# Optimization experiments

Hardware: AMD Instinct MI355X
Metric: run time of the kernel (lower is better)

The kernel has to match this reference:

```python
import jax, jax.numpy as jnp
import numpy as np

B, S, DM = 1, 4096, 2048
H, HD = 16, 128
TS = 16          # tile_size
TOPK = 16        # anchor tiles per query
NUM_TILES = S // TS


def setup_inputs() -> dict:
    key = jax.random.key(0)
    ks = jax.random.split(key, 7)
    x = jax.random.normal(ks[0], (B, S, DM), jnp.float32)
    Wq = jax.random.normal(ks[1], (DM, H * HD), jnp.float32) * 0.02
    Wk = jax.random.normal(ks[2], (DM, H * HD), jnp.float32) * 0.02
    Wv = jax.random.normal(ks[3], (DM, H * HD), jnp.float32) * 0.02
    Wo = jax.random.normal(ks[4], (H * HD, DM), jnp.float32) * 0.02
    # RoPE angles: pos * inv_freq, shape [S, HD//2] (= freqs_cis angle)
    inv_freq = 1.0 / (10000.0 ** (np.arange(0, HD, 2, dtype=np.float32) / HD))
    freqs = jnp.asarray(np.arange(S, dtype=np.float32)[:, None] * inv_freq[None, :])
    anchor_indices = jax.random.randint(ks[5], (B, H, S, TOPK), 0, NUM_TILES).astype(jnp.int32)
    return {"x": x, "Wq": Wq, "Wk": Wk, "Wv": Wv, "Wo": Wo,
            "freqs": freqs, "anchor_indices": anchor_indices}


def _rotate_half(z):
    half = z.shape[-1] // 2
    return jnp.concatenate([-z[..., half:], z[..., :half]], axis=-1)


def reference(x, Wq, Wk, Wv, Wo, freqs, anchor_indices):
    b, s, _ = x.shape
    num_tiles = s // TS
    # QKV projections -> [B, H, S, HD]
    q = (x @ Wq).reshape(b, s, H, HD).transpose(0, 2, 1, 3)
    k = (x @ Wk).reshape(b, s, H, HD).transpose(0, 2, 1, 3)
    v = (x @ Wv).reshape(b, s, H, HD).transpose(0, 2, 1, 3)
    # RoPE (half-split / rotate_half convention), float32
    cos = jnp.cos(freqs)[None, None, :s, :]
    sin = jnp.sin(freqs)[None, None, :s, :]
    cos_full = jnp.concatenate([cos, cos], axis=-1)
    sin_full = jnp.concatenate([sin, sin], axis=-1)
    q = q * cos_full + _rotate_half(q) * sin_full
    k = k * cos_full + _rotate_half(k) * sin_full
    # Per-query tile indices: anchor tiles + local tile
    local_tiles = (jnp.arange(s) // TS).astype(jnp.int32)
    local = jnp.broadcast_to(local_tiles[None, None, :, None], (b, H, s, 1))
    tiles = jnp.concatenate([anchor_indices, local], axis=-1)  # [B,H,S,K+1]
    # Representative query per tile (last token of each query tile)
    tile_repr = jnp.arange(TS - 1, s, TS)
    tile_sel = tiles[:, :, tile_repr, :]                        # [B,H,T,K+1]
    # Expand tile indices to token indices
    offsets = jnp.arange(TS)
    token_idx = tile_sel[..., None] * TS + offsets              # [B,H,T,K+1,TS]
    sparse_len = tile_sel.shape[-1] * TS
    flat_idx = jnp.clip(token_idx.reshape(b, H, num_tiles, sparse_len), 0, s - 1)
    # Gather sparse K/V per (batch, head, query-tile)
    k_flat = k.reshape(b * H, s, HD)
    v_flat = v.reshape(b * H, s, HD)
    idx_flat = flat_idx.reshape(b * H, num_tiles, sparse_len)
    k_sparse = jax.vmap(lambda kv, idx: kv[idx])(k_flat, idx_flat)
    v_sparse = jax.vmap(lambda kv, idx: kv[idx])(v_flat, idx_flat)
    k_sparse = k_sparse.reshape(b, H, num_tiles, sparse_len, HD)
    v_sparse = v_sparse.reshape(b, H, num_tiles, sparse_len, HD)
    # Block-sparse attention per tile
    q_tiled = q.reshape(b, H, num_tiles, TS, HD)
    logits = jnp.einsum('bhtqd,bhtkd->bhtqk', q_tiled, k_sparse) / jnp.sqrt(HD)
    q_pos = jnp.arange(s).reshape(num_tiles, TS)
    future_mask = flat_idx[:, :, :, None, :] > q_pos[None, None, :, :, None]
    logits = jnp.where(future_mask, -1e10, logits)
    weights = jax.nn.softmax(logits, axis=-1)
    all_masked = jnp.all(future_mask, axis=-1, keepdims=True)
    weights = jnp.where(all_masked, 0.0, weights)
    weights = jnp.where(jnp.isnan(weights), 0.0, weights)
    out = jnp.einsum('bhtqk,bhtkd->bhtqd', weights, v_sparse)
    out = out.reshape(b, H, s, HD).transpose(0, 2, 1, 3).reshape(b, s, H * HD)
    return out @ Wo
```

## Files before the change

### kernel.cpp

```cpp
#include <hip/hip_runtime.h>

typedef unsigned short u16;
typedef unsigned int u32;
typedef __attribute__((ext_vector_type(8))) short bf16x8;
typedef __attribute__((ext_vector_type(4))) float f32x4;

__device__ __forceinline__ u16 f2bf(float f) {
  union { float f; u32 u; } v; v.f = f;
  u32 u = v.u;
  return (u16)((u + 0x7FFFu + ((u >> 16) & 1u)) >> 16);
}
__device__ __forceinline__ float bf2f(u16 s) {
  union { u32 u; float f; } v; v.u = ((u32)s) << 16;
  return v.f;
}

__device__ __forceinline__ void async16(const void* g, void* l) {
  __builtin_amdgcn_global_load_lds(
      (__attribute__((address_space(1))) void*)g,
      (__attribute__((address_space(3))) void*)l, 16, 0, 0);
}

__global__ void cast4_kernel(const float* __restrict__ in, u16* __restrict__ out, int n4) {
  int i = blockIdx.x * 256 + threadIdx.x;
  if (i < n4) {
    float4 v = ((const float4*)in)[i];
    ushort4 o;
    o.x = f2bf(v.x); o.y = f2bf(v.y); o.z = f2bf(v.z); o.w = f2bf(v.w);
    ((ushort4*)out)[i] = o;
  }
}

__global__ void transpose_cast_kernel(const float* __restrict__ in, u16* __restrict__ out,
                                      int R, int C) {
  __shared__ float tile[32][33];
  int c0 = blockIdx.x * 32, r0 = blockIdx.y * 32;
  int tx = threadIdx.x, ty = threadIdx.y;
#pragma unroll
  for (int i = ty; i < 32; i += 8) tile[i][tx] = in[(size_t)(r0 + i) * C + c0 + tx];
  __syncthreads();
#pragma unroll
  for (int i = ty; i < 32; i += 8)
    out[(size_t)(c0 + i) * R + r0 + tx] = f2bf(tile[tx][i]);
}

__global__ void trig_kernel(const float* __restrict__ freqs, float* __restrict__ ct,
                            float* __restrict__ st, int n) {
  int i = blockIdx.x * 256 + threadIdx.x;
  if (i < n) { float f = freqs[i]; ct[i] = cosf(f); st[i] = sinf(f); }
}

__global__ void rope_kernel(u16* __restrict__ q, u16* __restrict__ k,
                            const float* __restrict__ ct, const float* __restrict__ st) {
  int i = blockIdx.x * 256 + threadIdx.x;
  int dp = (i & 31) * 2;
  int hh = (i >> 5) & 15;
  int s  = i >> 9;
  float c0 = ct[s * 64 + dp], c1 = ct[s * 64 + dp + 1];
  float s0 = st[s * 64 + dp], s1 = st[s * 64 + dp + 1];
  size_t base = (size_t)s * 2048 + hh * 128 + dp;
  {
    u32 lo = *(u32*)(q + base);
    u32 hi = *(u32*)(q + base + 64);
    float a0 = bf2f((u16)lo), a1 = bf2f((u16)(lo >> 16));
    float b0 = bf2f((u16)hi), b1 = bf2f((u16)(hi >> 16));
    u32 nlo = (u32)f2bf(a0 * c0 - b0 * s0) | ((u32)f2bf(a1 * c1 - b1 * s1) << 16);
    u32 nhi = (u32)f2bf(b0 * c0 + a0 * s0) | ((u32)f2bf(b1 * c1 + a1 * s1) << 16);
    *(u32*)(q + base) = nlo;
    *(u32*)(q + base + 64) = nhi;
  }
  {
    u32 lo = *(u32*)(k + base);
    u32 hi = *(u32*)(k + base + 64);
    float a0 = bf2f((u16)lo), a1 = bf2f((u16)(lo >> 16));
    float b0 = bf2f((u16)hi), b1 = bf2f((u16)(hi >> 16));
    u32 nlo = (u32)f2bf(a0 * c0 - b0 * s0) | ((u32)f2bf(a1 * c1 - b1 * s1) << 16);
    u32 nhi = (u32)f2bf(b0 * c0 + a0 * s0) | ((u32)f2bf(b1 * c1 + a1 * s1) << 16);
    *(u32*)(k + base) = nlo;
    *(u32*)(k + base + 64) = nhi;
  }
}

__global__ void repack_k_kernel(const u16* __restrict__ Kin, u16* __restrict__ Kp) {
  const int h = blockIdx.y;
  const int s0 = blockIdx.x * 64;
  const int tid = threadIdx.x;
#pragma unroll
  for (int i = 0; i < 16; ++i) {
    int idx = i * 256 + tid;
    int r = idx >> 6;
    int d2 = idx & 63;
    u32 kv = ((const u32*)Kin)[(size_t)(s0 + r) * 1024 + h * 64 + d2];
    ((u32*)Kp)[((size_t)h * 4096 + s0 + r) * 64 + d2] = kv;
  }
}

__global__ void repack_v_kernel(const u16* __restrict__ Vin, u16* __restrict__ VT2) {
  const int h = blockIdx.y;
  const int s0 = blockIdx.x * 64;
  const int tid = threadIdx.x;
  __shared__ u16 lv[64][132];
#pragma unroll
  for (int i = 0; i < 16; ++i) {
    int idx = i * 256 + tid;
    int r = idx >> 6;
    int d2 = idx & 63;
    u32 vv = ((const u32*)Vin)[(size_t)(s0 + r) * 1024 + h * 64 + d2];
    *(u32*)(&lv[r][d2 * 2]) = vv;
  }
  __syncthreads();
#pragma unroll
  for (int i = 0; i < 16; ++i) {
    int idx = i * 256 + tid;
    int k2 = idx & 7;
    int d  = (idx >> 3) & 127;
    int tl = idx >> 10;
    u32 lo = lv[tl * 16 + k2 * 2][d];
    u32 hi = lv[tl * 16 + k2 * 2 + 1][d];
    ((u32*)VT2)[(((size_t)h * 256 + blockIdx.x * 4 + tl) * 128 + d) * 8 + k2] = lo | (hi << 16);
  }
}

template <int OUTBF>
__launch_bounds__(256, 2)
__global__ void gemm128_kernel(const u16* __restrict__ A, const u16* __restrict__ Bt,
                               void* __restrict__ C, int M, int N, int K) {
  __shared__ __align__(16) u16 As[128 * 64];
  __shared__ __align__(16) u16 Bs[128 * 64];
  const int tid  = threadIdx.x;
  const int lane = tid & 63;
  const int wave = tid >> 6;
  const int wr = wave >> 1, wc = wave & 1;
  const int brow = blockIdx.y * 128;
  const int bcol = blockIdx.x * 128;

  int a_goff[4], b_goff[4], l_off[4];
#pragma unroll
  for (int i = 0; i < 4; ++i) {
    int p = (wave * 4 + i) * 1024 + lane * 16;
    int row = p >> 7;
    int colb = (p & 127) ^ ((row & 7) << 4);
    a_goff[i] = (brow + row) * K + (colb >> 1);
    b_goff[i] = (bcol + row) * K + (colb >> 1);
    l_off[i] = p;
  }

  f32x4 acc[4][4];
#pragma unroll
  for (int m = 0; m < 4; ++m)
#pragma unroll
    for (int n = 0; n < 4; ++n) acc[m][n] = (f32x4){0.f, 0.f, 0.f, 0.f};

  for (int k0 = 0; k0 < K; k0 += 64) {
#pragma unroll
    for (int i = 0; i < 4; ++i) {
      async16(A + a_goff[i] + k0, (char*)As + l_off[i]);
      async16(Bt + b_goff[i] + k0, (char*)Bs + l_off[i]);
    }
    __syncthreads();
#pragma unroll
    for (int kk = 0; kk < 2; ++kk) {
      bf16x8 af[4], bfr[4];
#pragma unroll
      for (int m = 0; m < 4; ++m) {
        int row = wr * 64 + m * 16 + (lane & 15);
        int byte = (row << 7) + ((kk * 64 + ((lane >> 4) << 4)) ^ ((row & 7) << 4));
        af[m] = *(const bf16x8*)((const char*)As + byte);
      }
#pragma unroll
      for (int n = 0; n < 4; ++n) {
        int row = wc * 64 + n * 16 + (lane & 15);
        int byte = (row << 7) + ((kk * 64 + ((lane >> 4) << 4)) ^ ((row & 7) << 4));
        bfr[n] = *(const bf16x8*)((const char*)Bs + byte);
      }
#pragma unroll
      for (int m = 0; m < 4; ++m)
#pragma unroll
        for (int n = 0; n < 4; ++n)
          acc[m][n] = __builtin_amdgcn_mfma_f32_16x16x32_bf16(af[m], bfr[n], acc[m][n], 0, 0, 0);
    }
    __syncthreads();
  }

  const int r0 = brow + wr * 64;
  const int c0 = bcol + wc * 64;
#pragma unroll
  for (int m = 0; m < 4; ++m)
#pragma unroll
    for (int n = 0; n < 4; ++n)
#pragma unroll
      for (int r = 0; r < 4; ++r) {
        int rr = r0 + m * 16 + ((lane >> 4) << 2) + r;
        int cc = c0 + n * 16 + (lane & 15);
        if (OUTBF) ((u16*)C)[(size_t)rr * N + cc] = f2bf(acc[m][n][r]);
        else       ((float*)C)[(size_t)rr * N + cc] = acc[m][n][r];
      }
}

__launch_bounds__(256, 3)
__global__ void attn_kernel(const u16* __restrict__ Q, const u16* __restrict__ Kp,
                            const u16* __restrict__ VT2, const int* __restrict__ anchors,
                            u16* __restrict__ Out) {
  const int t = blockIdx.x;
  const int h = blockIdx.y;
  __shared__ int tiles[18];
  __shared__ float lg[16][292];
  __shared__ __align__(16) u16 w_lds[16][296];
  const int tid  = threadIdx.x;
  const int lane = tid & 63;
  const int wave = tid >> 6;
  const int g = lane >> 4;
  const int c = lane & 15;

  if (tid < 16) tiles[tid] = anchors[(size_t)((h << 12) + (t * 16 + 15)) * 16 + tid];
  if (tid == 16) tiles[16] = t;
  if (tid == 17) tiles[17] = 0;
  __syncthreads();

  {
    const u16* qbase = Q + (size_t)(t * 16 + c) * 2048 + h * 128 + g * 8;
    bf16x8 qf[4];
#pragma unroll
    for (int ks = 0; ks < 4; ++ks) qf[ks] = *(const bf16x8*)(qbase + ks * 32);
    for (int j = wave; j < 17; j += 4) {
      int tok = tiles[j] * 16 + c;
      const u16* kbase = Kp + ((size_t)h * 4096 + tok) * 128 + g * 8;
      f32x4 a = (f32x4){0.f, 0.f, 0.f, 0.f};
#pragma unroll
      for (int ks = 0; ks < 4; ++ks) {
        bf16x8 kf = *(const bf16x8*)(kbase + ks * 32);
        a = __builtin_amdgcn_mfma_f32_16x16x32_bf16(qf[ks], kf, a, 0, 0, 0);
      }
#pragma unroll
      for (int r = 0; r < 4; ++r) {
        int qrow = g * 4 + r;
        float vv = a[r] * 0.088388347648318447f;
        if (tok > t * 16 + qrow) vv = -1e10f;
        lg[qrow][j * 16 + c] = vv;
      }
    }
  }
  __syncthreads();

  {
    const int r = tid >> 4, cc = tid & 15;
    float vals[17];
    float mx = -3.0e38f;
#pragma unroll
    for (int i = 0; i < 17; ++i) { vals[i] = lg[r][i * 16 + cc]; mx = fmaxf(mx, vals[i]); }
#pragma unroll
    for (int d = 1; d < 16; d <<= 1) mx = fmaxf(mx, __shfl_xor(mx, d, 64));
    float sum = 0.f;
#pragma unroll
    for (int i = 0; i < 17; ++i) { vals[i] = __expf(vals[i] - mx); sum += vals[i]; }
#pragma unroll
    for (int d = 1; d < 16; d <<= 1) sum += __shfl_xor(sum, d, 64);
    float inv = sum > 0.f ? 1.0f / sum : 0.f;
#pragma unroll
    for (int i = 0; i < 17; ++i) w_lds[r][i * 16 + cc] = f2bf(vals[i] * inv);
    w_lds[r][272 + cc] = 0;
  }
  __syncthreads();

  {
    f32x4 o0 = (f32x4){0.f, 0.f, 0.f, 0.f}, o1 = o0;
    const int d0 = wave * 32;
    const size_t hb = (size_t)h * 256;
    const int keyin = (g & 1) * 8;
#pragma unroll
    for (int ks = 0; ks < 9; ++ks) {
      bf16x8 af = *(const bf16x8*)(&w_lds[c][ks * 32 + g * 8]);
      int jt = 2 * ks + (g >> 1);
      const u16* vb = VT2 + (hb + tiles[jt]) * 128 * 16;
      bf16x8 b0 = *(const bf16x8*)(vb + (d0 + c) * 16 + keyin);
      bf16x8 b1 = *(const bf16x8*)(vb + (d0 + 16 + c) * 16 + keyin);
      o0 = __builtin_amdgcn_mfma_f32_16x16x32_bf16(af, b0, o0, 0, 0, 0);
      o1 = __builtin_amdgcn_mfma_f32_16x16x32_bf16(af, b1, o1, 0, 0, 0);
    }
#pragma unroll
    for (int r = 0; r < 4; ++r) {
      int qrow = g * 4 + r;
      size_t base = (size_t)(t * 16 + qrow) * 2048 + h * 128;
      Out[base + d0 + c]      = f2bf(o0[r]);
      Out[base + d0 + 16 + c] = f2bf(o1[r]);
    }
  }
}

extern "C" void kernel_launch(void* const* d_in, const int* in_sizes, int n_in,
                              void* d_out, int out_size, void* d_ws, size_t ws_size,
                              hipStream_t stream) {
  (void)in_sizes; (void)n_in; (void)out_size; (void)ws_size;
  const float* x      = (const float*)d_in[0];
  const float* Wq     = (const float*)d_in[1];
  const float* Wk     = (const float*)d_in[2];
  const float* Wv     = (const float*)d_in[3];
  const float* Wo     = (const float*)d_in[4];
  const float* Wo_f   = (const float*)d_in[4];
  const float* freqs  = (const float*)d_in[5];
  const int* anchors  = (const int*)d_in[6];
  (void)Wo_f;
  float* out = (float*)d_out;

  char* ws = (char*)d_ws;
  const size_t MB = 1024 * 1024;
  u16* xbf   = (u16*)(ws + 0);
  u16* wqT   = (u16*)(ws + 16 * MB);
  u16* wkT   = (u16*)(ws + 24 * MB);
  u16* wvT   = (u16*)(ws + 32 * MB);
  u16* woT   = (u16*)(ws + 40 * MB);
  u16* qbf   = (u16*)(ws + 48 * MB);
  u16* kbf   = (u16*)(ws + 64 * MB);
  u16* vbf   = (u16*)(ws + 80 * MB);
  u16* attnb = (u16*)(ws + 0);
  u16* Kp    = (u16*)(ws + 16 * MB);
  float* ct  = (float*)(ws + 32 * MB);
  float* st  = (float*)(ws + 33 * MB);
  u16* VT2   = (u16*)(ws + 64 * MB);

  cast4_kernel<<<8192, 256, 0, stream>>>(x, xbf, 2097152);
  dim3 tb(32, 8), tg(64, 64);
  transpose_cast_kernel<<<tg, tb, 0, stream>>>(Wq, wqT, 2048, 2048);
  transpose_cast_kernel<<<tg, tb, 0, stream>>>(Wk, wkT, 2048, 2048);
  transpose_cast_kernel<<<tg, tb, 0, stream>>>(Wv, wvT, 2048, 2048);
  transpose_cast_kernel<<<tg, tb, 0, stream>>>(Wo, woT, 2048, 2048);

  dim3 gg(16, 32);
  gemm128_kernel<1><<<gg, 256, 0, stream>>>(xbf, wqT, qbf, 4096, 2048, 2048);
  gemm128_kernel<1><<<gg, 256, 0, stream>>>(xbf, wkT, kbf, 4096, 2048, 2048);
  gemm128_kernel<1><<<gg, 256, 0, stream>>>(xbf, wvT, vbf, 4096, 2048, 2048);
  trig_kernel<<<1024, 256, 0, stream>>>(freqs, ct, st, 262144);
  rope_kernel<<<8192, 256, 0, stream>>>(qbf, kbf, ct, st);
  repack_k_kernel<<<dim3(64, 16), 256, 0, stream>>>(kbf, Kp);
  repack_v_kernel<<<dim3(64, 16), 256, 0, stream>>>(vbf, VT2);
  attn_kernel<<<dim3(256, 16), 256, 0, stream>>>(qbf, Kp, VT2, anchors, attnb);
  gemm128_kernel<0><<<gg, 256, 0, stream>>>(attnb, woT, out, 4096, 2048, 2048);
}
```

Measured before the change: 280.7 us.

## Fuse QKV GEMMs and weight transposes, fold K repack into RoPE, prefetch attention loads

The four weight transpose-casts now run as one launch over a z-dimension. The three QKV projections become one 6144-wide GEMM whose epilogue routes each column block to the Q, K or V buffer. RoPE writes rotated K straight into the head-major packed layout, so the separate K repack kernel is gone. The attention kernel double-buffers K and V fragment loads in registers and raises its occupancy bound to 4. Together these cut launch count, extra memory passes and load latency, at the cost of more register pressure in attention.

```diff
diff --git a/kernel.cpp b/kernel.cpp
--- a/kernel.cpp
+++ b/kernel.cpp
@@ -31,8 +31,14 @@
   }
 }
 
-__global__ void transpose_cast_kernel(const float* __restrict__ in, u16* __restrict__ out,
-                                      int R, int C) {
+__global__ void transpose_cast4_kernel(const float* __restrict__ W0, const float* __restrict__ W1,
+                                       const float* __restrict__ W2, const float* __restrict__ W3,
+                                       u16* __restrict__ O0, u16* __restrict__ O1,
+                                       u16* __restrict__ O2, u16* __restrict__ O3) {
+  const int R = 2048, C = 2048;
+  const int z = blockIdx.z;
+  const float* in = z == 0 ? W0 : z == 1 ? W1 : z == 2 ? W2 : W3;
+  u16* out = z == 0 ? O0 : z == 1 ? O1 : z == 2 ? O2 : O3;
   __shared__ float tile[32][33];
   int c0 = blockIdx.x * 32, r0 = blockIdx.y * 32;
   int tx = threadIdx.x, ty = threadIdx.y;
@@ -50,7 +56,8 @@
   if (i < n) { float f = freqs[i]; ct[i] = cosf(f); st[i] = sinf(f); }
 }
 
-__global__ void rope_kernel(u16* __restrict__ q, u16* __restrict__ k,
+__global__ void rope_kernel(u16* __restrict__ q, const u16* __restrict__ k,
+                            u16* __restrict__ Kp,
                             const float* __restrict__ ct, const float* __restrict__ st) {
   int i = blockIdx.x * 256 + threadIdx.x;
   int dp = (i & 31) * 2;
@@ -70,28 +77,15 @@
     *(u32*)(q + base + 64) = nhi;
   }
   {
-    u32 lo = *(u32*)(k + base);
-    u32 hi = *(u32*)(k + base + 64);
+    u32 lo = *(const u32*)(k + base);
+    u32 hi = *(const u32*)(k + base + 64);
     float a0 = bf2f((u16)lo), a1 = bf2f((u16)(lo >> 16));
     float b0 = bf2f((u16)hi), b1 = bf2f((u16)(hi >> 16));
     u32 nlo = (u32)f2bf(a0 * c0 - b0 * s0) | ((u32)f2bf(a1 * c1 - b1 * s1) << 16);
     u32 nhi = (u32)f2bf(b0 * c0 + a0 * s0) | ((u32)f2bf(b1 * c1 + a1 * s1) << 16);
-    *(u32*)(k + base) = nlo;
-    *(u32*)(k + base + 64) = nhi;
-  }
-}
-
-__global__ void repack_k_kernel(const u16* __restrict__ Kin, u16* __restrict__ Kp) {
-  const int h = blockIdx.y;
-  const int s0 = blockIdx.x * 64;
-  const int tid = threadIdx.x;
-#pragma unroll
-  for (int i = 0; i < 16; ++i) {
-    int idx = i * 256 + tid;
-    int r = idx >> 6;
-    int d2 = idx & 63;
-    u32 kv = ((const u32*)Kin)[(size_t)(s0 + r) * 1024 + h * 64 + d2];
-    ((u32*)Kp)[((size_t)h * 4096 + s0 + r) * 64 + d2] = kv;
+    size_t kpb = ((size_t)hh * 4096 + s) * 128 + dp;
+    *(u32*)(Kp + kpb) = nlo;
+    *(u32*)(Kp + kpb + 64) = nhi;
   }
 }
 
@@ -121,10 +115,11 @@
   }
 }
 
-template <int OUTBF>
+template <int MODE>
 __launch_bounds__(256, 2)
 __global__ void gemm128_kernel(const u16* __restrict__ A, const u16* __restrict__ Bt,
-                               void* __restrict__ C, int M, int N, int K) {
+                               void* __restrict__ C, u16* __restrict__ D1, u16* __restrict__ D2,
+                               int M, int N, int K) {
   __shared__ __align__(16) u16 As[128 * 64];
   __shared__ __align__(16) u16 Bs[128 * 64];
   const int tid  = threadIdx.x;
@@ -184,26 +179,42 @@
 
   const int r0 = brow + wr * 64;
   const int c0 = bcol + wc * 64;
-#pragma unroll
-  for (int m = 0; m < 4; ++m)
-#pragma unroll
-    for (int n = 0; n < 4; ++n)
-#pragma unroll
-      for (int r = 0; r < 4; ++r) {
-        int rr = r0 + m * 16 + ((lane >> 4) << 2) + r;
-        int cc = c0 + n * 16 + (lane & 15);
-        if (OUTBF) ((u16*)C)[(size_t)rr * N + cc] = f2bf(acc[m][n][r]);
-        else       ((float*)C)[(size_t)rr * N + cc] = acc[m][n][r];
-      }
-}
-
-__launch_bounds__(256, 3)
+  if (MODE == 2) {
+    const int sel = bcol >> 11;
+    u16* dst = sel == 0 ? (u16*)C : sel == 1 ? D1 : D2;
+    const int c0l = (bcol & 2047) + wc * 64;
+#pragma unroll
+    for (int m = 0; m < 4; ++m)
+#pragma unroll
+      for (int n = 0; n < 4; ++n)
+#pragma unroll
+        for (int r = 0; r < 4; ++r) {
+          int rr = r0 + m * 16 + ((lane >> 4) << 2) + r;
+          int cc = c0l + n * 16 + (lane & 15);
+          dst[(size_t)rr * 2048 + cc] = f2bf(acc[m][n][r]);
+        }
+  } else {
+#pragma unroll
+    for (int m = 0; m < 4; ++m)
+#pragma unroll
+      for (int n = 0; n < 4; ++n)
+#pragma unroll
+        for (int r = 0; r < 4; ++r) {
+          int rr = r0 + m * 16 + ((lane >> 4) << 2) + r;
+          int cc = c0 + n * 16 + (lane & 15);
+          if (MODE == 1) ((u16*)C)[(size_t)rr * N + cc] = f2bf(acc[m][n][r]);
+          else           ((float*)C)[(size_t)rr * N + cc] = acc[m][n][r];
+        }
+  }
+}
+
+__launch_bounds__(256, 4)
 __global__ void attn_kernel(const u16* __restrict__ Q, const u16* __restrict__ Kp,
                             const u16* __restrict__ VT2, const int* __restrict__ anchors,
                             u16* __restrict__ Out) {
   const int t = blockIdx.x;
   const int h = blockIdx.y;
-  __shared__ int tiles[18];
+  __shared__ int tiles[20];
   __shared__ float lg[16][292];
   __shared__ __align__(16) u16 w_lds[16][296];
   const int tid  = threadIdx.x;
@@ -214,7 +225,7 @@
 
   if (tid < 16) tiles[tid] = anchors[(size_t)((h << 12) + (t * 16 + 15)) * 16 + tid];
   if (tid == 16) tiles[16] = t;
-  if (tid == 17) tiles[17] = 0;
+  if (tid >= 17 && tid < 20) tiles[tid] = 0;
   __syncthreads();
 
   {
@@ -222,21 +233,38 @@
     bf16x8 qf[4];
 #pragma unroll
     for (int ks = 0; ks < 4; ++ks) qf[ks] = *(const bf16x8*)(qbase + ks * 32);
-    for (int j = wave; j < 17; j += 4) {
-      int tok = tiles[j] * 16 + c;
-      const u16* kbase = Kp + ((size_t)h * 4096 + tok) * 128 + g * 8;
+
+    int tok_[5];
+    const u16* kb_[5];
+#pragma unroll
+    for (int i = 0; i < 5; ++i) {
+      int j = wave + 4 * i;
+      tok_[i] = tiles[j] * 16 + c;
+      kb_[i] = Kp + ((size_t)h * 4096 + tok_[i]) * 128 + g * 8;
+    }
+    bf16x8 kfp[2][4];
+#pragma unroll
+    for (int ks = 0; ks < 4; ++ks) kfp[0][ks] = *(const bf16x8*)(kb_[0] + ks * 32);
+#pragma unroll
+    for (int i = 0; i < 5; ++i) {
+      if (i < 4) {
+#pragma unroll
+        for (int ks = 0; ks < 4; ++ks)
+          kfp[(i + 1) & 1][ks] = *(const bf16x8*)(kb_[i + 1] + ks * 32);
+      }
       f32x4 a = (f32x4){0.f, 0.f, 0.f, 0.f};
 #pragma unroll
-      for (int ks = 0; ks < 4; ++ks) {
-        bf16x8 kf = *(const bf16x8*)(kbase + ks * 32);
-        a = __builtin_amdgcn_mfma_f32_16x16x32_bf16(qf[ks], kf, a, 0, 0, 0);
-      }
-#pragma unroll
-      for (int r = 0; r < 4; ++r) {
-        int qrow = g * 4 + r;
-        float vv = a[r] * 0.088388347648318447f;
-        if (tok > t * 16 + qrow) vv = -1e10f;
-        lg[qrow][j * 16 + c] = vv;
+      for (int ks = 0; ks < 4; ++ks)
+        a = __builtin_amdgcn_mfma_f32_16x16x32_bf16(qf[ks], kfp[i & 1][ks], a, 0, 0, 0);
+      int j = wave + 4 * i;
+      if (j < 17) {
+#pragma unroll
+        for (int r = 0; r < 4; ++r) {
+          int qrow = g * 4 + r;
+          float vv = a[r] * 0.088388347648318447f;
+          if (tok_[i] > t * 16 + qrow) vv = -1e10f;
+          lg[qrow][j * 16 + c] = vv;
+        }
       }
     }
   }
@@ -267,15 +295,21 @@
     const int d0 = wave * 32;
     const size_t hb = (size_t)h * 256;
     const int keyin = (g & 1) * 8;
+    const u16* vb_[9];
+#pragma unroll
+    for (int ks = 0; ks < 9; ++ks) vb_[ks] = VT2 + (hb + tiles[2 * ks + (g >> 1)]) * 2048;
+    bf16x8 pb0[2], pb1[2];
+    pb0[0] = *(const bf16x8*)(vb_[0] + (d0 + c) * 16 + keyin);
+    pb1[0] = *(const bf16x8*)(vb_[0] + (d0 + 16 + c) * 16 + keyin);
 #pragma unroll
     for (int ks = 0; ks < 9; ++ks) {
+      if (ks < 8) {
+        pb0[(ks + 1) & 1] = *(const bf16x8*)(vb_[ks + 1] + (d0 + c) * 16 + keyin);
+        pb1[(ks + 1) & 1] = *(const bf16x8*)(vb_[ks + 1] + (d0 + 16 + c) * 16 + keyin);
+      }
       bf16x8 af = *(const bf16x8*)(&w_lds[c][ks * 32 + g * 8]);
-      int jt = 2 * ks + (g >> 1);
-      const u16* vb = VT2 + (hb + tiles[jt]) * 128 * 16;
-      bf16x8 b0 = *(const bf16x8*)(vb + (d0 + c) * 16 + keyin);
-      bf16x8 b1 = *(const bf16x8*)(vb + (d0 + 16 + c) * 16 + keyin);
-      o0 = __builtin_amdgcn_mfma_f32_16x16x32_bf16(af, b0, o0, 0, 0, 0);
-      o1 = __builtin_amdgcn_mfma_f32_16x16x32_bf16(af, b1, o1, 0, 0, 0);
+      o0 = __builtin_amdgcn_mfma_f32_16x16x32_bf16(af, pb0[ks & 1], o0, 0, 0, 0);
+      o1 = __builtin_amdgcn_mfma_f32_16x16x32_bf16(af, pb1[ks & 1], o1, 0, 0, 0);
     }
 #pragma unroll
     for (int r = 0; r < 4; ++r) {
@@ -296,18 +330,14 @@
   const float* Wk     = (const float*)d_in[2];
   const float* Wv     = (const float*)d_in[3];
   const float* Wo     = (const float*)d_in[4];
-  const float* Wo_f   = (const float*)d_in[4];
   const float* freqs  = (const float*)d_in[5];
   const int* anchors  = (const int*)d_in[6];
-  (void)Wo_f;
   float* out = (float*)d_out;
 
   char* ws = (char*)d_ws;
   const size_t MB = 1024 * 1024;
   u16* xbf   = (u16*)(ws + 0);
-  u16* wqT   = (u16*)(ws + 16 * MB);
-  u16* wkT   = (u16*)(ws + 24 * MB);
-  u16* wvT   = (u16*)(ws + 32 * MB);
+  u16* wqkvT = (u16*)(ws + 16 * MB);
   u16* woT   = (u16*)(ws + 40 * MB);
   u16* qbf   = (u16*)(ws + 48 * MB);
   u16* kbf   = (u16*)(ws + 64 * MB);
@@ -319,20 +349,17 @@
   u16* VT2   = (u16*)(ws + 64 * MB);
 
   cast4_kernel<<<8192, 256, 0, stream>>>(x, xbf, 2097152);
-  dim3 tb(32, 8), tg(64, 64);
-  transpose_cast_kernel<<<tg, tb, 0, stream>>>(Wq, wqT, 2048, 2048);
-  transpose_cast_kernel<<<tg, tb, 0, stream>>>(Wk, wkT, 2048, 2048);
-  transpose_cast_kernel<<<tg, tb, 0, stream>>>(Wv, wvT, 2048, 2048);
-  transpose_cast_kernel<<<tg, tb, 0, stream>>>(Wo, woT, 2048, 2048);
-
-  dim3 gg(16, 32);
-  gemm128_kernel<1><<<gg, 256, 0, stream>>>(xbf, wqT, qbf, 4096, 2048, 2048);
-  gemm128_kernel<1><<<gg, 256, 0, stream>>>(xbf, wkT, kbf, 4096, 2048, 2048);
-  gemm128_kernel<1><<<gg, 256, 0, stream>>>(xbf, wvT, vbf, 4096, 2048, 2048);
+  dim3 tb(32, 8), tg4(64, 64, 4);
+  transpose_cast4_kernel<<<tg4, tb, 0, stream>>>(
+      Wq, Wk, Wv, Wo,
+      wqkvT, wqkvT + (size_t)8 * MB / 2, wqkvT + (size_t)16 * MB / 2, woT);
+
+  gemm128_kernel<2><<<dim3(48, 32), 256, 0, stream>>>(xbf, wqkvT, qbf, kbf, vbf,
+                                                      4096, 6144, 2048);
   trig_kernel<<<1024, 256, 0, stream>>>(freqs, ct, st, 262144);
-  rope_kernel<<<8192, 256, 0, stream>>>(qbf, kbf, ct, st);
-  repack_k_kernel<<<dim3(64, 16), 256, 0, stream>>>(kbf, Kp);
+  rope_kernel<<<8192, 256, 0, stream>>>(qbf, kbf, Kp, ct, st);
   repack_v_kernel<<<dim3(64, 16), 256, 0, stream>>>(vbf, VT2);
   attn_kernel<<<dim3(256, 16), 256, 0, stream>>>(qbf, Kp, VT2, anchors, attnb);
-  gemm128_kernel<0><<<gg, 256, 0, stream>>>(attnb, woT, out, 4096, 2048, 2048);
-}
+  gemm128_kernel<0><<<dim3(16, 32), 256, 0, stream>>>(attnb, woT, out, nullptr, nullptr,
+                                                      4096, 2048, 2048);
+}
```

After: 251.9 us. -10.3%, faster.
